# Kernel optimization log

Hardware: AMD Instinct MI355X
Metric: run time of the kernel (lower is better)

Reference implementation:

```python
import jax, jax.numpy as jnp
import numpy as np

B, S, DM, H = 16, 512, 256, 8
DF = DM // H          # per-head feature dim
K_INDEX = 5           # keep top-(K_INDEX) probs per row (SparseKT soft-threshold top-k)
NEG_MASK = -1e32      # fill for causal mask
NEG_SPARSE = -1e16    # fill for sub-threshold probs before re-softmax


def setup_inputs() -> dict:
    key = jax.random.key(0)
    ks = jax.random.split(key, 6)
    sc = 1.0 / np.sqrt(DM)  # ~xavier scale
    q = jax.random.normal(ks[0], (B, S, DM), jnp.float32)
    k = jax.random.normal(ks[1], (B, S, DM), jnp.float32)
    v = jax.random.normal(ks[2], (B, S, DM), jnp.float32)
    # causal lower-triangular mask, [1,1,S,S]; scores where mask==0 -> -1e32
    mask = jnp.tril(jnp.ones((S, S), jnp.int32))[None, None]
    # k_linear / v_linear / out_proj weights (key_query_same=True -> q shares k_linear)
    Wk = jax.random.normal(ks[3], (DM, DM), jnp.float32) * sc
    Wv = jax.random.normal(ks[4], (DM, DM), jnp.float32) * sc
    Wo = jax.random.normal(ks[5], (DM, DM), jnp.float32) * sc
    bk = jnp.zeros((DM,), jnp.float32)
    bv = jnp.zeros((DM,), jnp.float32)
    bo = jnp.zeros((DM,), jnp.float32)
    return {"q": q, "k": k, "v": v, "mask": mask, "zero_pad": 1,
            "Wk": Wk, "bk": bk, "Wv": Wv, "bv": bv, "Wo": Wo, "bo": bo}


def _heads(x, W, b):
    # Linear then split heads: [B,S,DM] -> [B,H,S,DF]
    y = x @ W.T + b
    return y.reshape(B, S, H, DF).transpose(0, 2, 1, 3)


def reference(q, k, v, mask, zero_pad, Wk, bk, Wv, bv, Wo, bo):
    qh = _heads(q, Wk, bk)  # key_query_same: q uses k_linear
    kh = _heads(k, Wk, bk)
    vh = _heads(v, Wv, bv)

    scores = jnp.einsum("bhqd,bhkd->bhqk", qh, kh) / np.sqrt(DF)
    scores = jnp.where(mask == 0, jnp.float32(NEG_MASK), scores)
    attn = jax.nn.softmax(scores, axis=-1)

    if K_INDEX + 1 < S:
        attn_a = attn[:, :, : K_INDEX + 1, :]          # short rows kept as-is
        attn_b = attn[:, :, K_INDEX + 1 :, :]          # rows to sparsify
        # threshold = K_INDEX-th largest prob per row (== sorted desc [k_index-1])
        thr = jax.lax.top_k(attn_b, K_INDEX)[0][..., -1:]
        attn_b = jnp.where(attn_b - thr >= 0, attn_b, jnp.float32(NEG_SPARSE))
        attn_b = jax.nn.softmax(attn_b, axis=-1)
        attn = jnp.concatenate([attn_a, attn_b], axis=2)

    if zero_pad:
        attn = jnp.concatenate(
            [jnp.zeros_like(attn[:, :, :1, :]), attn[:, :, 1:, :]], axis=2)

    # dropout is identity in eval mode
    ctx = jnp.einsum("bhqk,bhkd->bhqd", attn, vh)
    concat = ctx.transpose(0, 2, 1, 3).reshape(B, S, DM)
    output = concat @ Wo.T + bo
    return output, attn
```

## Files before the change

kernel.cpp:

```cpp
#include <hip/hip_runtime.h>
#include <hip/hip_bf16.h>
#include <math.h>

#define BB 16
#define SS 512
#define DMM 256
#define HH 8
#define DFF 32
#define KIDX 5

__device__ __forceinline__ void gemm_body(
    const float* __restrict__ X, const float* __restrict__ W,
    const float* __restrict__ bias, float* __restrict__ Y, const bool heads)
{
  __shared__ float As[16][64];
  __shared__ float Bs[16][64];
  const int tid = threadIdx.x;
  const int tx = tid & 15;
  const int ty = (tid >> 4) & 15;
  const int m0 = blockIdx.x * 64;
  const int n0 = blockIdx.y * 64;
  const int r  = tid >> 2;
  const int c4 = (tid & 3) << 2;

  float4 ax = *reinterpret_cast<const float4*>(&X[(size_t)(m0 + r) * DMM + c4]);
  float4 wx = *reinterpret_cast<const float4*>(&W[(size_t)(n0 + r) * DMM + c4]);
  float acc[4][4] = {};

  for (int k0 = 0; k0 < DMM; k0 += 16) {
    As[c4 + 0][r] = ax.x; As[c4 + 1][r] = ax.y; As[c4 + 2][r] = ax.z; As[c4 + 3][r] = ax.w;
    Bs[c4 + 0][r] = wx.x; Bs[c4 + 1][r] = wx.y; Bs[c4 + 2][r] = wx.z; Bs[c4 + 3][r] = wx.w;
    __syncthreads();
    if (k0 + 16 < DMM) {
      ax = *reinterpret_cast<const float4*>(&X[(size_t)(m0 + r) * DMM + k0 + 16 + c4]);
      wx = *reinterpret_cast<const float4*>(&W[(size_t)(n0 + r) * DMM + k0 + 16 + c4]);
    }
    #pragma unroll
    for (int kk = 0; kk < 16; ++kk) {
      const float4 a4 = *reinterpret_cast<const float4*>(&As[kk][ty * 4]);
      const float4 b4 = *reinterpret_cast<const float4*>(&Bs[kk][tx * 4]);
      acc[0][0] += a4.x * b4.x; acc[0][1] += a4.x * b4.y; acc[0][2] += a4.x * b4.z; acc[0][3] += a4.x * b4.w;
      acc[1][0] += a4.y * b4.x; acc[1][1] += a4.y * b4.y; acc[1][2] += a4.y * b4.z; acc[1][3] += a4.y * b4.w;
      acc[2][0] += a4.z * b4.x; acc[2][1] += a4.z * b4.y; acc[2][2] += a4.z * b4.z; acc[2][3] += a4.z * b4.w;
      acc[3][0] += a4.w * b4.x; acc[3][1] += a4.w * b4.y; acc[3][2] += a4.w * b4.z; acc[3][3] += a4.w * b4.w;
    }
    __syncthreads();
  }
  #pragma unroll
  for (int i = 0; i < 4; ++i) {
    const int m = m0 + ty * 4 + i;
    #pragma unroll
    for (int j = 0; j < 4; ++j) {
      const int n = n0 + tx * 4 + j;
      const float v = acc[i][j] + bias[n];
      if (heads) {
        const int b = m >> 9;
        const int s = m & (SS - 1);
        const int h = n >> 5;
        const int d = n & (DFF - 1);
        Y[(((size_t)b * HH + h) * SS + s) * DFF + d] = v;
      } else {
        Y[(size_t)m * DMM + n] = v;
      }
    }
  }
}

__global__ __launch_bounds__(256) void proj_kernel(
    const float* __restrict__ q, const float* __restrict__ k, const float* __restrict__ v,
    const float* __restrict__ Wk, const float* __restrict__ bk,
    const float* __restrict__ Wv, const float* __restrict__ bv,
    float* __restrict__ qh, float* __restrict__ kh, float* __restrict__ vh)
{
  const int z = blockIdx.z;
  const float* X = (z == 0) ? q : (z == 1) ? k : v;
  const float* W = (z == 2) ? Wv : Wk;
  const float* bias = (z == 2) ? bv : bk;
  float* Y = (z == 0) ? qh : (z == 1) ? kh : vh;
  gemm_body(X, W, bias, Y, true);
}

__global__ __launch_bounds__(256) void out_kernel(
    const float* __restrict__ X, const float* __restrict__ Wo,
    const float* __restrict__ bo, float* __restrict__ Y)
{
  gemm_body(X, Wo, bo, Y, false);
}

__global__ __launch_bounds__(256) void attn_kernel(
    const float* __restrict__ qh,
    const float* __restrict__ kh,
    const float* __restrict__ vh,
    const int* __restrict__ zp,
    float* __restrict__ attn,
    float* __restrict__ concat)
{
  __shared__ float Ksh[DFF][64];
  __shared__ float ws_w[4][8];
  __shared__ int   ws_c[4][8];

  const int tid  = threadIdx.x;
  const int lane = tid & 63;
  const int wave = tid >> 6;
  const int grp  = blockIdx.x;
  const int bh   = grp >> 7;
  const int base = (grp & 127) << 2;
  const int qrow = base + wave;
  const int b    = bh >> 3;
  const int h    = bh & 7;
  const int ncols = qrow + 1;
  const float scale = 0.17677669529663688f;

  const float* kb = kh + (size_t)bh * SS * DFF;
  const float* vb = vh + (size_t)bh * SS * DFF;

  float qreg[DFF];
  {
    const float* qp = qh + ((size_t)bh * SS + qrow) * DFF;
    #pragma unroll
    for (int i = 0; i < DFF / 4; ++i) {
      const float4 t = *reinterpret_cast<const float4*>(qp + i * 4);
      qreg[i*4+0] = t.x; qreg[i*4+1] = t.y; qreg[i*4+2] = t.z; qreg[i*4+3] = t.w;
    }
  }

  const int nch  = ((base + 3) >> 6) + 1;
  const int mych = qrow >> 6;

  const int scol = tid & 63;
  const int sd0  = (tid >> 6) << 3;

  float p[8];
  #pragma unroll
  for (int i = 0; i < 8; ++i) p[i] = -INFINITY;

  const float* kp0 = kb + (size_t)scol * DFF + sd0;
  float4 r0 = *reinterpret_cast<const float4*>(kp0);
  float4 r1 = *reinterpret_cast<const float4*>(kp0 + 4);

  for (int c = 0; c < nch; ++c) {
    Ksh[sd0 + 0][scol] = r0.x; Ksh[sd0 + 1][scol] = r0.y;
    Ksh[sd0 + 2][scol] = r0.z; Ksh[sd0 + 3][scol] = r0.w;
    Ksh[sd0 + 4][scol] = r1.x; Ksh[sd0 + 5][scol] = r1.y;
    Ksh[sd0 + 6][scol] = r1.z; Ksh[sd0 + 7][scol] = r1.w;
    __syncthreads();
    if (c + 1 < nch) {
      const float* kp = kb + (size_t)(((c + 1) << 6) + scol) * DFF + sd0;
      r0 = *reinterpret_cast<const float4*>(kp);
      r1 = *reinterpret_cast<const float4*>(kp + 4);
    }
    if (c <= mych) {
      const int col = (c << 6) + lane;
      float da = 0.f, db = 0.f;
      #pragma unroll
      for (int d = 0; d < DFF; d += 2) {
        da += Ksh[d    ][lane] * qreg[d];
        db += Ksh[d + 1][lane] * qreg[d + 1];
      }
      if (col < ncols) p[c] = (da + db) * scale;
    }
    __syncthreads();
  }

  float m = p[0];
  #pragma unroll
  for (int s2 = 1; s2 < 8; ++s2) m = fmaxf(m, p[s2]);
  #pragma unroll
  for (int off = 32; off >= 1; off >>= 1) m = fmaxf(m, __shfl_xor(m, off, 64));
  float sum = 0.f;
  #pragma unroll
  for (int s2 = 0; s2 < 8; ++s2) {
    const float e = (p[s2] == -INFINITY) ? 0.f : expf(p[s2] - m);
    p[s2] = e;
    sum += e;
  }
  #pragma unroll
  for (int off = 32; off >= 1; off >>= 1) sum += __shfl_xor(sum, off, 64);
  const float inv = 1.0f / sum;
  #pragma unroll
  for (int s2 = 0; s2 < 8; ++s2) p[s2] *= inv;

  float neww[8];
  if (qrow > KIDX) {
    float pv[8];
    #pragma unroll
    for (int s2 = 0; s2 < 8; ++s2) {
      const int col = lane + (s2 << 6);
      pv[s2] = (col < ncols) ? p[s2] : -INFINITY;
    }
    float thr = 0.f, m1 = 0.f;
    #pragma unroll
    for (int t = 0; t < KIDX; ++t) {
      float bv = -INFINITY;
      int   bi = 0x7fffffff;
      #pragma unroll
      for (int s2 = 0; s2 < 8; ++s2) {
        if (pv[s2] > bv) { bv = pv[s2]; bi = lane + (s2 << 6); }
      }
      #pragma unroll
      for (int off = 32; off >= 1; off >>= 1) {
        const float ov = __shfl_xor(bv, off, 64);
        const int   oi = __shfl_xor(bi, off, 64);
        if (ov > bv || (ov == bv && oi < bi)) { bv = ov; bi = oi; }
      }
      if (t == 0) m1 = bv;
      thr = bv;
      const int osl = bi >> 6;
      if ((bi & 63) == lane) {
        #pragma unroll
        for (int s2 = 0; s2 < 8; ++s2) if (s2 == osl) pv[s2] = -INFINITY;
      }
    }
    float nsum = 0.f;
    #pragma unroll
    for (int s2 = 0; s2 < 8; ++s2) {
      const int col = lane + (s2 << 6);
      float e = 0.f;
      if (col < ncols && (p[s2] - thr >= 0.f)) e = expf(p[s2] - m1);
      neww[s2] = e;
      nsum += e;
    }
    #pragma unroll
    for (int off = 32; off >= 1; off >>= 1) nsum += __shfl_xor(nsum, off, 64);
    const float ninv = 1.0f / nsum;
    #pragma unroll
    for (int s2 = 0; s2 < 8; ++s2) neww[s2] *= ninv;
  } else {
    #pragma unroll
    for (int s2 = 0; s2 < 8; ++s2) neww[s2] = p[s2];
  }

  if (qrow == 0 && *zp != 0) {
    #pragma unroll
    for (int s2 = 0; s2 < 8; ++s2) neww[s2] = 0.f;
  }

  {
    float* arow = attn + ((size_t)bh * SS + qrow) * SS;
    #pragma unroll
    for (int s2 = 0; s2 < 8; ++s2) arow[lane + (s2 << 6)] = neww[s2];
  }

  {
    unsigned long long msks[8];
    #pragma unroll
    for (int s2 = 0; s2 < 8; ++s2) msks[s2] = __ballot(neww[s2] != 0.f);
    int rbase = 0;
    #pragma unroll
    for (int s2 = 0; s2 < 8; ++s2) {
      const unsigned long long msk = msks[s2];
      const int myr = rbase + __popcll(msk & ((1ull << lane) - 1ull));
      if (((msk >> lane) & 1ull) && myr < 8) {
        ws_w[wave][myr] = neww[s2];
        ws_c[wave][myr] = (s2 << 6) | lane;
      }
      rbase += __popcll(msk);
    }
    const int nk = rbase;
    if (lane < 8 && lane >= nk) { ws_w[wave][lane] = 0.f; ws_c[wave][lane] = 0; }

    const int dd = lane & 31;
    float accv = 0.f;
    if (nk <= 8) {
      #pragma unroll
      for (int i = 0; i < 8; ++i)
        accv += ws_w[wave][i] * vb[(size_t)ws_c[wave][i] * DFF + dd];
    } else {
      #pragma unroll
      for (int s2 = 0; s2 < 8; ++s2) {
        unsigned long long msk = msks[s2];
        while (msk) {
          const int src = __ffsll(msk) - 1;
          msk &= msk - 1;
          accv += __shfl(neww[s2], src, 64) * vb[(size_t)(src + (s2 << 6)) * DFF + dd];
        }
      }
    }
    if (lane < 32)
      concat[((size_t)b * SS + qrow) * DMM + h * DFF + dd] = accv;
  }
}

extern "C" void kernel_launch(void* const* d_in, const int* in_sizes, int n_in,
                              void* d_out, int out_size, void* d_ws, size_t ws_size,
                              hipStream_t stream) {
  const float* q  = (const float*)d_in[0];
  const float* k  = (const float*)d_in[1];
  const float* v  = (const float*)d_in[2];
  const int*   zp = (const int*)d_in[4];
  const float* Wk = (const float*)d_in[5];
  const float* bk = (const float*)d_in[6];
  const float* Wv = (const float*)d_in[7];
  const float* bv = (const float*)d_in[8];
  const float* Wo = (const float*)d_in[9];
  const float* bo = (const float*)d_in[10];

  float* ws     = (float*)d_ws;
  float* qhp    = ws;
  float* khp    = ws + 2097152;
  float* vhp    = ws + 4194304;
  float* concat = ws + 6291456;

  float* outp  = (float*)d_out;
  float* attnp = outp + (size_t)BB * SS * DMM;

  proj_kernel<<<dim3(128, 4, 3), 256, 0, stream>>>(q, k, v, Wk, bk, Wv, bv, qhp, khp, vhp);
  attn_kernel<<<dim3(BB * HH * SS / 4), 256, 0, stream>>>(qhp, khp, vhp, zp, attnp, concat);
  out_kernel<<<dim3(128, 4), 256, 0, stream>>>(concat, Wo, bo, outp);
}
```

Baseline: 348.1 us.

## Retile projection GEMMs, swizzle K tile, and use sorting-network top-k

```diff
diff --git a/kernel.cpp b/kernel.cpp
--- a/kernel.cpp
+++ b/kernel.cpp
@@ -9,59 +9,95 @@
 #define DFF 32
 #define KIDX 5
 
+template<int TM, bool HEADS>
 __device__ __forceinline__ void gemm_body(
     const float* __restrict__ X, const float* __restrict__ W,
-    const float* __restrict__ bias, float* __restrict__ Y, const bool heads)
+    const float* __restrict__ bias, float* __restrict__ Y)
 {
-  __shared__ float As[16][64];
-  __shared__ float Bs[16][64];
+  constexpr int RM = TM / 16;
+  constexpr int NA = TM / 32;
+  __shared__ float As[32][TM];
+  __shared__ float Bs[32][64];
   const int tid = threadIdx.x;
   const int tx = tid & 15;
-  const int ty = (tid >> 4) & 15;
-  const int m0 = blockIdx.x * 64;
+  const int ty = tid >> 4;
+  const int m0 = blockIdx.x * TM;
   const int n0 = blockIdx.y * 64;
-  const int r  = tid >> 2;
-  const int c4 = (tid & 3) << 2;
-
-  float4 ax = *reinterpret_cast<const float4*>(&X[(size_t)(m0 + r) * DMM + c4]);
-  float4 wx = *reinterpret_cast<const float4*>(&W[(size_t)(n0 + r) * DMM + c4]);
-  float acc[4][4] = {};
-
-  for (int k0 = 0; k0 < DMM; k0 += 16) {
-    As[c4 + 0][r] = ax.x; As[c4 + 1][r] = ax.y; As[c4 + 2][r] = ax.z; As[c4 + 3][r] = ax.w;
-    Bs[c4 + 0][r] = wx.x; Bs[c4 + 1][r] = wx.y; Bs[c4 + 2][r] = wx.z; Bs[c4 + 3][r] = wx.w;
+
+  float4 pa[NA], pb[2];
+  #pragma unroll
+  for (int i = 0; i < NA; ++i) {
+    const int f = tid * NA + i;
+    pa[i] = *reinterpret_cast<const float4*>(&X[(size_t)(m0 + (f >> 3)) * DMM + ((f & 7) << 2)]);
+  }
+  #pragma unroll
+  for (int i = 0; i < 2; ++i) {
+    const int f = tid * 2 + i;
+    pb[i] = *reinterpret_cast<const float4*>(&W[(size_t)(n0 + (f >> 3)) * DMM + ((f & 7) << 2)]);
+  }
+
+  float acc[RM][4] = {};
+
+  for (int k0 = 0; k0 < DMM; k0 += 32) {
+    #pragma unroll
+    for (int i = 0; i < NA; ++i) {
+      const int f = tid * NA + i;
+      const int ar = f >> 3, ac4 = (f & 7) << 2;
+      As[ac4 + 0][ar] = pa[i].x; As[ac4 + 1][ar] = pa[i].y;
+      As[ac4 + 2][ar] = pa[i].z; As[ac4 + 3][ar] = pa[i].w;
+    }
+    #pragma unroll
+    for (int i = 0; i < 2; ++i) {
+      const int f = tid * 2 + i;
+      const int br = f >> 3, bc4 = (f & 7) << 2;
+      Bs[bc4 + 0][br] = pb[i].x; Bs[bc4 + 1][br] = pb[i].y;
+      Bs[bc4 + 2][br] = pb[i].z; Bs[bc4 + 3][br] = pb[i].w;
+    }
     __syncthreads();
-    if (k0 + 16 < DMM) {
-      ax = *reinterpret_cast<const float4*>(&X[(size_t)(m0 + r) * DMM + k0 + 16 + c4]);
-      wx = *reinterpret_cast<const float4*>(&W[(size_t)(n0 + r) * DMM + k0 + 16 + c4]);
-    }
-    #pragma unroll
-    for (int kk = 0; kk < 16; ++kk) {
-      const float4 a4 = *reinterpret_cast<const float4*>(&As[kk][ty * 4]);
+    if (k0 + 32 < DMM) {
+      #pragma unroll
+      for (int i = 0; i < NA; ++i) {
+        const int f = tid * NA + i;
+        pa[i] = *reinterpret_cast<const float4*>(&X[(size_t)(m0 + (f >> 3)) * DMM + k0 + 32 + ((f & 7) << 2)]);
+      }
+      #pragma unroll
+      for (int i = 0; i < 2; ++i) {
+        const int f = tid * 2 + i;
+        pb[i] = *reinterpret_cast<const float4*>(&W[(size_t)(n0 + (f >> 3)) * DMM + k0 + 32 + ((f & 7) << 2)]);
+      }
+    }
+    #pragma unroll
+    for (int kk = 0; kk < 32; ++kk) {
       const float4 b4 = *reinterpret_cast<const float4*>(&Bs[kk][tx * 4]);
-      acc[0][0] += a4.x * b4.x; acc[0][1] += a4.x * b4.y; acc[0][2] += a4.x * b4.z; acc[0][3] += a4.x * b4.w;
-      acc[1][0] += a4.y * b4.x; acc[1][1] += a4.y * b4.y; acc[1][2] += a4.y * b4.z; acc[1][3] += a4.y * b4.w;
-      acc[2][0] += a4.z * b4.x; acc[2][1] += a4.z * b4.y; acc[2][2] += a4.z * b4.z; acc[2][3] += a4.z * b4.w;
-      acc[3][0] += a4.w * b4.x; acc[3][1] += a4.w * b4.y; acc[3][2] += a4.w * b4.z; acc[3][3] += a4.w * b4.w;
+      #pragma unroll
+      for (int r4 = 0; r4 < RM / 4; ++r4) {
+        const float4 a4 = *reinterpret_cast<const float4*>(&As[kk][ty * RM + r4 * 4]);
+        const int i0 = r4 * 4;
+        acc[i0+0][0] += a4.x * b4.x; acc[i0+0][1] += a4.x * b4.y; acc[i0+0][2] += a4.x * b4.z; acc[i0+0][3] += a4.x * b4.w;
+        acc[i0+1][0] += a4.y * b4.x; acc[i0+1][1] += a4.y * b4.y; acc[i0+1][2] += a4.y * b4.z; acc[i0+1][3] += a4.y * b4.w;
+        acc[i0+2][0] += a4.z * b4.x; acc[i0+2][1] += a4.z * b4.y; acc[i0+2][2] += a4.z * b4.z; acc[i0+2][3] += a4.z * b4.w;
+        acc[i0+3][0] += a4.w * b4.x; acc[i0+3][1] += a4.w * b4.y; acc[i0+3][2] += a4.w * b4.z; acc[i0+3][3] += a4.w * b4.w;
+      }
     }
     __syncthreads();
   }
-  #pragma unroll
-  for (int i = 0; i < 4; ++i) {
-    const int m = m0 + ty * 4 + i;
-    #pragma unroll
-    for (int j = 0; j < 4; ++j) {
-      const int n = n0 + tx * 4 + j;
-      const float v = acc[i][j] + bias[n];
-      if (heads) {
-        const int b = m >> 9;
-        const int s = m & (SS - 1);
-        const int h = n >> 5;
-        const int d = n & (DFF - 1);
-        Y[(((size_t)b * HH + h) * SS + s) * DFF + d] = v;
-      } else {
-        Y[(size_t)m * DMM + n] = v;
-      }
+
+  const int n = n0 + tx * 4;
+  const float4 b4 = *reinterpret_cast<const float4*>(&bias[n]);
+  #pragma unroll
+  for (int i = 0; i < RM; ++i) {
+    const int m = m0 + ty * RM + i;
+    float4 o;
+    o.x = acc[i][0] + b4.x; o.y = acc[i][1] + b4.y;
+    o.z = acc[i][2] + b4.z; o.w = acc[i][3] + b4.w;
+    if (HEADS) {
+      const int b = m >> 9;
+      const int s = m & (SS - 1);
+      const int h = n >> 5;
+      const int d = n & (DFF - 1);
+      *reinterpret_cast<float4*>(&Y[(((size_t)b * HH + h) * SS + s) * DFF + d]) = o;
+    } else {
+      *reinterpret_cast<float4*>(&Y[(size_t)m * DMM + n]) = o;
     }
   }
 }
@@ -77,14 +113,14 @@
   const float* W = (z == 2) ? Wv : Wk;
   const float* bias = (z == 2) ? bv : bk;
   float* Y = (z == 0) ? qh : (z == 1) ? kh : vh;
-  gemm_body(X, W, bias, Y, true);
+  gemm_body<128, true>(X, W, bias, Y);
 }
 
 __global__ __launch_bounds__(256) void out_kernel(
     const float* __restrict__ X, const float* __restrict__ Wo,
     const float* __restrict__ bo, float* __restrict__ Y)
 {
-  gemm_body(X, Wo, bo, Y, false);
+  gemm_body<64, false>(X, Wo, bo, Y);
 }
 
 __global__ __launch_bounds__(256) void attn_kernel(
@@ -95,7 +131,7 @@
     float* __restrict__ attn,
     float* __restrict__ concat)
 {
-  __shared__ float Ksh[DFF][64];
+  __shared__ float4 Ksh[64 * 8];
   __shared__ float ws_w[4][8];
   __shared__ int   ws_c[4][8];
 
@@ -114,50 +150,51 @@
   const float* kb = kh + (size_t)bh * SS * DFF;
   const float* vb = vh + (size_t)bh * SS * DFF;
 
-  float qreg[DFF];
+  float4 q4[8];
   {
     const float* qp = qh + ((size_t)bh * SS + qrow) * DFF;
     #pragma unroll
-    for (int i = 0; i < DFF / 4; ++i) {
-      const float4 t = *reinterpret_cast<const float4*>(qp + i * 4);
-      qreg[i*4+0] = t.x; qreg[i*4+1] = t.y; qreg[i*4+2] = t.z; qreg[i*4+3] = t.w;
-    }
+    for (int g = 0; g < 8; ++g)
+      q4[g] = *reinterpret_cast<const float4*>(qp + g * 4);
   }
 
   const int nch  = ((base + 3) >> 6) + 1;
   const int mych = qrow >> 6;
 
   const int scol = tid & 63;
-  const int sd0  = (tid >> 6) << 3;
+  const int g0   = (tid >> 6) << 1;
 
   float p[8];
   #pragma unroll
   for (int i = 0; i < 8; ++i) p[i] = -INFINITY;
 
-  const float* kp0 = kb + (size_t)scol * DFF + sd0;
+  const float* kp0 = kb + (size_t)scol * DFF + g0 * 4;
   float4 r0 = *reinterpret_cast<const float4*>(kp0);
   float4 r1 = *reinterpret_cast<const float4*>(kp0 + 4);
 
   for (int c = 0; c < nch; ++c) {
-    Ksh[sd0 + 0][scol] = r0.x; Ksh[sd0 + 1][scol] = r0.y;
-    Ksh[sd0 + 2][scol] = r0.z; Ksh[sd0 + 3][scol] = r0.w;
-    Ksh[sd0 + 4][scol] = r1.x; Ksh[sd0 + 5][scol] = r1.y;
-    Ksh[sd0 + 6][scol] = r1.z; Ksh[sd0 + 7][scol] = r1.w;
+    Ksh[(scol << 3) + ((g0 + scol) & 7)]     = r0;
+    Ksh[(scol << 3) + ((g0 + 1 + scol) & 7)] = r1;
     __syncthreads();
     if (c + 1 < nch) {
-      const float* kp = kb + (size_t)(((c + 1) << 6) + scol) * DFF + sd0;
+      const float* kp = kb + (size_t)(((c + 1) << 6) + scol) * DFF + g0 * 4;
       r0 = *reinterpret_cast<const float4*>(kp);
       r1 = *reinterpret_cast<const float4*>(kp + 4);
     }
     if (c <= mych) {
       const int col = (c << 6) + lane;
-      float da = 0.f, db = 0.f;
-      #pragma unroll
-      for (int d = 0; d < DFF; d += 2) {
-        da += Ksh[d    ][lane] * qreg[d];
-        db += Ksh[d + 1][lane] * qreg[d + 1];
-      }
-      if (col < ncols) p[c] = (da + db) * scale;
+      float d0 = 0.f, d1 = 0.f;
+      #pragma unroll
+      for (int g = 0; g < 8; ++g) {
+        const int pg = (g + lane) & 7;
+        const float4 kv = Ksh[(lane << 3) + pg];
+        const float4 qv = q4[g];
+        d0 = fmaf(qv.x, kv.x, d0);
+        d1 = fmaf(qv.y, kv.y, d1);
+        d0 = fmaf(qv.z, kv.z, d0);
+        d1 = fmaf(qv.w, kv.w, d1);
+      }
+      if (col < ncols) p[c] = (d0 + d1) * scale;
     }
     __syncthreads();
   }
@@ -170,7 +207,7 @@
   float sum = 0.f;
   #pragma unroll
   for (int s2 = 0; s2 < 8; ++s2) {
-    const float e = (p[s2] == -INFINITY) ? 0.f : expf(p[s2] - m);
+    const float e = (p[s2] == -INFINITY) ? 0.f : __expf(p[s2] - m);
     p[s2] = e;
     sum += e;
   }
@@ -182,41 +219,46 @@
 
   float neww[8];
   if (qrow > KIDX) {
-    float pv[8];
+    float v[8];
     #pragma unroll
     for (int s2 = 0; s2 < 8; ++s2) {
       const int col = lane + (s2 << 6);
-      pv[s2] = (col < ncols) ? p[s2] : -INFINITY;
-    }
-    float thr = 0.f, m1 = 0.f;
-    #pragma unroll
-    for (int t = 0; t < KIDX; ++t) {
-      float bv = -INFINITY;
-      int   bi = 0x7fffffff;
-      #pragma unroll
-      for (int s2 = 0; s2 < 8; ++s2) {
-        if (pv[s2] > bv) { bv = pv[s2]; bi = lane + (s2 << 6); }
-      }
-      #pragma unroll
-      for (int off = 32; off >= 1; off >>= 1) {
-        const float ov = __shfl_xor(bv, off, 64);
-        const int   oi = __shfl_xor(bi, off, 64);
-        if (ov > bv || (ov == bv && oi < bi)) { bv = ov; bi = oi; }
-      }
-      if (t == 0) m1 = bv;
-      thr = bv;
-      const int osl = bi >> 6;
-      if ((bi & 63) == lane) {
-        #pragma unroll
-        for (int s2 = 0; s2 < 8; ++s2) if (s2 == osl) pv[s2] = -INFINITY;
-      }
-    }
+      v[s2] = (col < ncols) ? p[s2] : -INFINITY;
+    }
+    #define CE(i, j) { const float t = fmaxf(v[i], v[j]); v[j] = fminf(v[i], v[j]); v[i] = t; }
+    CE(0,1) CE(2,3) CE(4,5) CE(6,7)
+    CE(0,2) CE(1,3) CE(4,6) CE(5,7)
+    CE(1,2) CE(5,6)
+    CE(0,4) CE(1,5) CE(2,6) CE(3,7)
+    CE(2,4) CE(3,5)
+    CE(1,2) CE(3,4) CE(5,6)
+    #undef CE
+    float a0 = v[0], a1 = v[1], a2 = v[2], a3 = v[3], a4 = v[4];
+    #pragma unroll
+    for (int off = 1; off <= 32; off <<= 1) {
+      const float b0 = __shfl_xor(a0, off, 64);
+      const float b1 = __shfl_xor(a1, off, 64);
+      const float b2 = __shfl_xor(a2, off, 64);
+      const float b3 = __shfl_xor(a3, off, 64);
+      const float b4 = __shfl_xor(a4, off, 64);
+      const float n0 = fmaxf(a0, b0);
+      const float n1 = fmaxf(fmaxf(a1, b1), fminf(a0, b0));
+      const float n2 = fmaxf(fmaxf(a2, b2), fmaxf(fminf(a0, b1), fminf(a1, b0)));
+      const float n3 = fmaxf(fmaxf(a3, b3),
+                       fmaxf(fmaxf(fminf(a0, b2), fminf(a1, b1)), fminf(a2, b0)));
+      const float n4 = fmaxf(fmaxf(a4, b4),
+                       fmaxf(fmaxf(fminf(a0, b3), fminf(a1, b2)),
+                             fmaxf(fminf(a2, b1), fminf(a3, b0))));
+      a0 = n0; a1 = n1; a2 = n2; a3 = n3; a4 = n4;
+    }
+    const float m1 = a0;
+    const float thr = a4;
     float nsum = 0.f;
     #pragma unroll
     for (int s2 = 0; s2 < 8; ++s2) {
       const int col = lane + (s2 << 6);
       float e = 0.f;
-      if (col < ncols && (p[s2] - thr >= 0.f)) e = expf(p[s2] - m1);
+      if (col < ncols && (p[s2] - thr >= 0.f)) e = __expf(p[s2] - m1);
       neww[s2] = e;
       nsum += e;
     }
@@ -304,7 +346,7 @@
   float* outp  = (float*)d_out;
   float* attnp = outp + (size_t)BB * SS * DMM;
 
-  proj_kernel<<<dim3(128, 4, 3), 256, 0, stream>>>(q, k, v, Wk, bk, Wv, bv, qhp, khp, vhp);
+  proj_kernel<<<dim3(64, 4, 3), 256, 0, stream>>>(q, k, v, Wk, bk, Wv, bv, qhp, khp, vhp);
   attn_kernel<<<dim3(BB * HH * SS / 4), 256, 0, stream>>>(qhp, khp, vhp, zp, attnp, concat);
   out_kernel<<<dim3(128, 4), 256, 0, stream>>>(concat, Wo, bo, outp);
 }
```

New measurement: 333.7 us. 4.1% less time.
